# Kernel optimization log

Hardware: AMD Instinct MI355X
Metric: run time of the kernel (lower is better)

## Reference

```python
import jax, jax.numpy as jnp
import numpy as np

N_NODES = 100000
N_GRAPHS = 64


def gcn_conv(x, edge_index, edge_weight, W, b):
    # PyG GCNConv: h = W^T x, then out[dst] += norm * h[src], norm = d^-1/2[src]*w*d^-1/2[dst]
    n = x.shape[0]
    loop = jnp.arange(n)
    src = jnp.concatenate([edge_index[0], loop])
    dst = jnp.concatenate([edge_index[1], loop])
    w = jnp.concatenate([edge_weight, jnp.ones((n,), x.dtype)])  # self-loop weight 1
    deg = jax.ops.segment_sum(w, dst, num_segments=n)
    dis = jnp.where(deg > 0, jax.lax.rsqrt(jnp.maximum(deg, 1e-30)), 0.0)
    norm = dis[src] * w * dis[dst]                      # [E+N]
    h = x @ W                                            # [N, d_out]
    msg = h[src] * norm[:, None]                         # gather + scale
    out = jax.ops.segment_sum(msg, dst, num_segments=n)  # scatter-add
    return out + b


def setup_inputs() -> dict:
    key = jax.random.key(0)
    k = jax.random.split(key, 8)
    d_in, d_out = 256, 128
    E = 1600000
    x = jax.random.normal(k[0], (N_NODES, d_in), jnp.float32)
    edge_index = jax.random.randint(k[1], (2, E), 0, N_NODES, jnp.int64)
    edge_weight = jax.random.uniform(k[2], (E,), jnp.float32)
    batch = jnp.sort(jax.random.randint(k[3], (N_NODES,), 0, N_GRAPHS, jnp.int64))
    W_conv = jax.random.normal(k[4], (d_in, d_out), jnp.float32) / np.sqrt(d_in)
    b_conv = jnp.zeros((d_out,), jnp.float32)
    W_lin = jax.random.normal(k[5], (d_out, 1), jnp.float32) / np.sqrt(d_out)
    b_lin = jnp.zeros((1,), jnp.float32)
    return {"x": x, "edge_index": edge_index, "edge_weight": edge_weight,
            "batch": batch, "W_conv": W_conv, "b_conv": b_conv,
            "W_lin": W_lin, "b_lin": b_lin}


def reference(x, edge_index, edge_weight, batch, W_conv, b_conv, W_lin, b_lin):
    h = gcn_conv(x, edge_index, edge_weight, W_conv, b_conv)
    h = jax.nn.relu(h)
    # dropout(p=0.1) treated as identity (eval) for deterministic baseline
    sums = jax.ops.segment_sum(h, batch, num_segments=N_GRAPHS)
    counts = jax.ops.segment_sum(jnp.ones((h.shape[0],), h.dtype), batch,
                                 num_segments=N_GRAPHS)
    pooled = sums / jnp.maximum(counts, 1.0)[:, None]    # [G, d_out]
    logits = pooled @ W_lin + b_lin                       # [G, 1]
    return jax.nn.sigmoid(logits)
```

## Files before the change

kernel.cpp:

```cpp
#include <hip/hip_runtime.h>
#include <hip/hip_bf16.h>
#include <math.h>

#define D_IN 256
#define D_OUT 128
#define WSCALE 1073741824.0f

typedef __bf16 bf16x8 __attribute__((ext_vector_type(8)));
typedef float  f32x4  __attribute__((ext_vector_type(4)));

__device__ __forceinline__ float b2f(ushort u) {
    union { unsigned int i; float f; } v; v.i = ((unsigned int)u) << 16; return v.f;
}
__device__ __forceinline__ ushort f2b(float f) {
    unsigned int x = __float_as_uint(f);
    unsigned int r = (x + 0x7FFFu + ((x >> 16) & 1u)) >> 16;
    return (ushort)r;
}

__global__ void edge_k(const int* __restrict__ dst, const float* __restrict__ w,
                       unsigned long long* __restrict__ packed,
                       int* __restrict__ pos, int E) {
    int e = blockIdx.x * blockDim.x + threadIdx.x;
    if (e >= E) return;
    int d = dst[e];
    unsigned long long inc = (1ull << 40) |
        (unsigned long long)(w[e] * WSCALE);
    unsigned long long old = atomicAdd(&packed[d], inc);
    pos[e] = (int)(old >> 40);
}

__global__ __launch_bounds__(256) void scan1_k(const unsigned long long* __restrict__ packed,
                                               int* __restrict__ row_start,
                                               int* __restrict__ blksum,
                                               float* __restrict__ dis, int N) {
    __shared__ int sdata[256];
    int t = threadIdx.x;
    int base = blockIdx.x * 1024;
    int v[4], s = 0;
    #pragma unroll
    for (int i = 0; i < 4; ++i) {
        int idx = base + t * 4 + i;
        if (idx < N) {
            unsigned long long p = packed[idx];
            v[i] = (int)(p >> 40);
            float deg = 1.0f + (float)(p & ((1ull << 40) - 1)) * (1.0f / WSCALE);
            dis[idx] = rsqrtf(deg);
        } else v[i] = 0;
        s += v[i];
    }
    sdata[t] = s;
    __syncthreads();
    #pragma unroll
    for (int off = 1; off < 256; off <<= 1) {
        int x = 0;
        if (t >= off) x = sdata[t - off];
        __syncthreads();
        sdata[t] += x;
        __syncthreads();
    }
    int excl = sdata[t] - s;
    if (t == 255) blksum[blockIdx.x] = sdata[t];
    int run = excl;
    #pragma unroll
    for (int i = 0; i < 4; ++i) {
        int idx = base + t * 4 + i;
        if (idx < N) row_start[idx] = run;
        run += v[i];
    }
}

__global__ __launch_bounds__(256) void scan2_k(const int* __restrict__ blksum,
                                               int* __restrict__ blkpre,
                                               int NB, int* __restrict__ row_start, int N) {
    __shared__ int s[256];
    int t = threadIdx.x;
    int v = (t < NB) ? blksum[t] : 0;
    s[t] = v;
    __syncthreads();
    #pragma unroll
    for (int off = 1; off < 256; off <<= 1) {
        int x = 0;
        if (t >= off) x = s[t - off];
        __syncthreads();
        s[t] += x;
        __syncthreads();
    }
    if (t < NB) blkpre[t] = s[t] - v;
    if (t == 255) row_start[N] = s[255];
}

__global__ void scan3_k(int* __restrict__ row_start, const int* __restrict__ blkpre, int N) {
    int idx = blockIdx.x * blockDim.x + threadIdx.x;
    if (idx < N) row_start[idx] += blkpre[idx >> 10];
}

__global__ void fill_k(const int* __restrict__ src, const int* __restrict__ dst,
                       const float* __restrict__ w, const int* __restrict__ pos,
                       const int* __restrict__ row_start,
                       int2* __restrict__ csr, int E) {
    int e = blockIdx.x * blockDim.x + threadIdx.x;
    if (e >= E) return;
    int d = dst[e];
    int2 rec;
    rec.x = src[e];
    rec.y = __float_as_int(w[e]);
    csr[row_start[d] + pos[e]] = rec;
}

__global__ void wt_k(const float* __restrict__ W, ushort* __restrict__ Wtg) {
    int t = blockIdx.x * 256 + threadIdx.x;
    if (t < D_IN * D_OUT) {
        int k = t >> 7, n = t & 127;
        Wtg[n * D_IN + k] = f2b(W[t]);
    }
}

__global__ __launch_bounds__(256, 2) void gemm_k(const float* __restrict__ X,
                                                 const ushort* __restrict__ Wtg,
                                                 const float* __restrict__ dis,
                                                 ushort* __restrict__ H, int M) {
    extern __shared__ char smem[];
    const int t = threadIdx.x;
    const int brow = blockIdx.x * 128;
    const int wid = t >> 6;
    const int lane = t & 63;
    const int lrow = lane & 15;
    const int lkc = lane >> 4;

    bf16x8 breg[2][8];
    #pragma unroll
    for (int n = 0; n < 2; ++n) {
        int col = wid * 32 + n * 16 + lrow;
        const char* base = (const char*)(Wtg + col * D_IN);
        #pragma unroll
        for (int kk = 0; kk < 8; ++kk)
            breg[n][kk] = *(const bf16x8*)(base + kk * 64 + lkc * 16);
    }

    {
        const float4* x4 = (const float4*)X;
        #pragma unroll
        for (int i = 0; i < 32; ++i) {
            int f = t + 256 * i;
            int row = f >> 6;
            int c4 = f & 63;
            int gr = brow + row;
            if (gr > M - 1) gr = M - 1;
            float4 v = x4[(size_t)gr * 64 + c4];
            ushort4 u;
            u.x = f2b(v.x); u.y = f2b(v.y); u.z = f2b(v.z); u.w = f2b(v.w);
            int phys = row * 512 + (((c4 >> 1) ^ (row & 7)) << 4) + ((c4 & 1) << 3);
            *(ushort4*)(smem + phys) = u;
        }
    }
    __syncthreads();

    f32x4 acc[8][2];
    #pragma unroll
    for (int m = 0; m < 8; ++m)
        #pragma unroll
        for (int n = 0; n < 2; ++n) acc[m][n] = (f32x4){0.f, 0.f, 0.f, 0.f};

    #pragma unroll
    for (int kk = 0; kk < 8; ++kk) {
        bf16x8 a[8];
        #pragma unroll
        for (int m = 0; m < 8; ++m) {
            int row = m * 16 + lrow;
            int chunk = kk * 4 + lkc;
            a[m] = *(const bf16x8*)(smem + row * 512 + ((chunk ^ (row & 7)) << 4));
        }
        #pragma unroll
        for (int m = 0; m < 8; ++m) {
            acc[m][0] = __builtin_amdgcn_mfma_f32_16x16x32_bf16(a[m], breg[0][kk], acc[m][0], 0, 0, 0);
            acc[m][1] = __builtin_amdgcn_mfma_f32_16x16x32_bf16(a[m], breg[1][kk], acc[m][1], 0, 0, 0);
        }
    }

    #pragma unroll
    for (int m = 0; m < 8; ++m) {
        #pragma unroll
        for (int v = 0; v < 4; ++v) {
            int gr = brow + m * 16 + lkc * 4 + v;
            if (gr < M) {
                float dsc = dis[gr];
                size_t rb = (size_t)gr * D_OUT;
                H[rb + wid * 32 + lrow]      = f2b(dsc * acc[m][0][v]);
                H[rb + wid * 32 + 16 + lrow] = f2b(dsc * acc[m][1][v]);
            }
        }
    }
}

__global__ __launch_bounds__(256) void agg_pool_k(const int* __restrict__ row_start,
                                                  const int2* __restrict__ csr,
                                                  const ushort* __restrict__ h,
                                                  const float* __restrict__ dis,
                                                  const float* __restrict__ bconv,
                                                  const int* __restrict__ batch,
                                                  float* __restrict__ pooled,
                                                  float* __restrict__ counts, int N) {
    int wave = threadIdx.x >> 6;
    int lane = threadIdx.x & 63;
    int c = lane * 2;
    float2 b2 = *(const float2*)&bconv[c];
    int base = blockIdx.x * 64 + wave;

    float2 accp = make_float2(0.f, 0.f);
    int curg = -1;
    float gcount = 0.f;

    #pragma unroll 1
    for (int i = 0; i < 16; ++i) {
        int n = base + 4 * i;
        if (n >= N) break;
        int rs = row_start[n];
        int re = row_start[n + 1];
        float din = dis[n];
        ushort2 hu = *(const ushort2*)&h[(size_t)n * D_OUT + c];
        float ax = b2f(hu.x);
        float ay = b2f(hu.y);
        int j = rs;
        for (; j + 3 < re; j += 4) {
            int2 r0 = csr[j];
            int2 r1 = csr[j + 1];
            int2 r2 = csr[j + 2];
            int2 r3 = csr[j + 3];
            ushort2 u0 = *(const ushort2*)&h[(size_t)r0.x * D_OUT + c];
            ushort2 u1 = *(const ushort2*)&h[(size_t)r1.x * D_OUT + c];
            ushort2 u2 = *(const ushort2*)&h[(size_t)r2.x * D_OUT + c];
            ushort2 u3 = *(const ushort2*)&h[(size_t)r3.x * D_OUT + c];
            float n0 = __int_as_float(r0.y), n1 = __int_as_float(r1.y);
            float n2 = __int_as_float(r2.y), n3 = __int_as_float(r3.y);
            ax += n0 * b2f(u0.x) + n1 * b2f(u1.x) + n2 * b2f(u2.x) + n3 * b2f(u3.x);
            ay += n0 * b2f(u0.y) + n1 * b2f(u1.y) + n2 * b2f(u2.y) + n3 * b2f(u3.y);
        }
        for (; j < re; ++j) {
            int2 r0 = csr[j];
            ushort2 u0 = *(const ushort2*)&h[(size_t)r0.x * D_OUT + c];
            float n0 = __int_as_float(r0.y);
            ax += n0 * b2f(u0.x);
            ay += n0 * b2f(u0.y);
        }
        float vx = fmaxf(din * ax + b2.x, 0.f);
        float vy = fmaxf(din * ay + b2.y, 0.f);
        int g = batch[n];
        if (g != curg) {
            if (curg >= 0) {
                atomicAdd(&pooled[curg * D_OUT + c],     accp.x);
                atomicAdd(&pooled[curg * D_OUT + c + 1], accp.y);
                if (lane == 0) atomicAdd(&counts[curg], gcount);
            }
            accp = make_float2(0.f, 0.f);
            gcount = 0.f;
            curg = g;
        }
        accp.x += vx;
        accp.y += vy;
        gcount += 1.f;
    }
    if (curg >= 0) {
        atomicAdd(&pooled[curg * D_OUT + c],     accp.x);
        atomicAdd(&pooled[curg * D_OUT + c + 1], accp.y);
        if (lane == 0) atomicAdd(&counts[curg], gcount);
    }
}

__global__ void head_k(const float* __restrict__ pooled, const float* __restrict__ counts,
                       const float* __restrict__ wlin, const float* __restrict__ blin,
                       float* __restrict__ out, int G) {
    int g = blockIdx.x;
    int lane = threadIdx.x;
    float s = 0.f;
    for (int c = lane; c < D_OUT; c += 64)
        s += pooled[g * D_OUT + c] * wlin[c];
    #pragma unroll
    for (int off = 32; off; off >>= 1) s += __shfl_down(s, off);
    if (lane == 0) {
        float cnt = fmaxf(counts[g], 1.0f);
        float z = s / cnt + blin[0];
        out[g] = 1.0f / (1.0f + expf(-z));
    }
}

extern "C" void kernel_launch(void* const* d_in, const int* in_sizes, int n_in,
                              void* d_out, int out_size, void* d_ws, size_t ws_size,
                              hipStream_t stream) {
    const float* x     = (const float*)d_in[0];
    const int*   ei    = (const int*)  d_in[1];
    const float* ew    = (const float*)d_in[2];
    const int*   batch = (const int*)  d_in[3];
    const float* Wc    = (const float*)d_in[4];
    const float* bc    = (const float*)d_in[5];
    const float* Wl    = (const float*)d_in[6];
    const float* bl    = (const float*)d_in[7];
    float* out = (float*)d_out;

    const int E = in_sizes[2];
    const int N = in_sizes[3];
    const int G = out_size;
    const int NB = (N + 1023) >> 10;

    const int* src = ei;
    const int* dst = ei + E;

    unsigned long long* packed = (unsigned long long*)d_ws;
    float*  pooled   = (float*)(packed + N);
    float*  counts   = pooled + (size_t)G * D_OUT;
    int*    pos      = (int*)(counts + G);
    float*  dis      = (float*)(pos + E);
    ushort* h        = (ushort*)(dis + N);
    ushort* Wtg      = h + (size_t)N * D_OUT;
    int2*   csr      = (int2*)(Wtg + D_IN * D_OUT);
    int*    row_start= (int*)(csr + E);
    int*    blksum   = row_start + N + 1;
    int*    blkpre   = blksum + NB;

    size_t zbytes = (size_t)N * 8 + ((size_t)G * D_OUT + G) * sizeof(float);
    hipMemsetAsync(packed, 0, zbytes, stream);

    edge_k    <<<(E + 255) / 256, 256, 0, stream>>>(dst, ew, packed, pos, E);

    scan1_k   <<<NB, 256, 0, stream>>>(packed, row_start, blksum, dis, N);
    scan2_k   <<<1, 256, 0, stream>>>(blksum, blkpre, NB, row_start, N);
    scan3_k   <<<(N + 255) / 256, 256, 0, stream>>>(row_start, blkpre, N);

    fill_k    <<<(E + 255) / 256, 256, 0, stream>>>(src, dst, ew, pos, row_start, csr, E);

    wt_k      <<<(D_IN * D_OUT + 255) / 256, 256, 0, stream>>>(Wc, Wtg);
    gemm_k    <<<(N + 127) / 128, 256, 65536, stream>>>(x, Wtg, dis, h, N);

    agg_pool_k<<<(N + 63) / 64, 256, 0, stream>>>(row_start, csr, h, dis, bc, batch, pooled, counts, N);

    head_k    <<<G, 64, 0, stream>>>(pooled, counts, Wl, bl, out, G);
}
```

Before: 261.8 us.

## Fuse edge-degree atomics with GEMM and precompute full edge norms in CSR

Merges the edge degree-counting kernel and the GEMM into one launch whose leading blocks do the atomics and whose trailing blocks do the matmul, so the two independent stages overlap. The GEMM no longer scales rows by dis. The full symmetric norm dis[src]*w*dis[dst] is instead computed in fill_k and stored in the CSR record, and the self-loop is scaled by dis^2. The aggregation kernel now gives each wave 16 contiguous nodes, which improves batch-segment locality, and its edge loop gathers 8 neighbours at a time with masked tails. Costs include the dropped min-2-blocks launch bound on the GEMM and extra random dis gathers in fill_k.

```diff
diff --git a/kernel.cpp b/kernel.cpp
--- a/kernel.cpp
+++ b/kernel.cpp
@@ -16,96 +16,6 @@
     unsigned int x = __float_as_uint(f);
     unsigned int r = (x + 0x7FFFu + ((x >> 16) & 1u)) >> 16;
     return (ushort)r;
-}
-
-__global__ void edge_k(const int* __restrict__ dst, const float* __restrict__ w,
-                       unsigned long long* __restrict__ packed,
-                       int* __restrict__ pos, int E) {
-    int e = blockIdx.x * blockDim.x + threadIdx.x;
-    if (e >= E) return;
-    int d = dst[e];
-    unsigned long long inc = (1ull << 40) |
-        (unsigned long long)(w[e] * WSCALE);
-    unsigned long long old = atomicAdd(&packed[d], inc);
-    pos[e] = (int)(old >> 40);
-}
-
-__global__ __launch_bounds__(256) void scan1_k(const unsigned long long* __restrict__ packed,
-                                               int* __restrict__ row_start,
-                                               int* __restrict__ blksum,
-                                               float* __restrict__ dis, int N) {
-    __shared__ int sdata[256];
-    int t = threadIdx.x;
-    int base = blockIdx.x * 1024;
-    int v[4], s = 0;
-    #pragma unroll
-    for (int i = 0; i < 4; ++i) {
-        int idx = base + t * 4 + i;
-        if (idx < N) {
-            unsigned long long p = packed[idx];
-            v[i] = (int)(p >> 40);
-            float deg = 1.0f + (float)(p & ((1ull << 40) - 1)) * (1.0f / WSCALE);
-            dis[idx] = rsqrtf(deg);
-        } else v[i] = 0;
-        s += v[i];
-    }
-    sdata[t] = s;
-    __syncthreads();
-    #pragma unroll
-    for (int off = 1; off < 256; off <<= 1) {
-        int x = 0;
-        if (t >= off) x = sdata[t - off];
-        __syncthreads();
-        sdata[t] += x;
-        __syncthreads();
-    }
-    int excl = sdata[t] - s;
-    if (t == 255) blksum[blockIdx.x] = sdata[t];
-    int run = excl;
-    #pragma unroll
-    for (int i = 0; i < 4; ++i) {
-        int idx = base + t * 4 + i;
-        if (idx < N) row_start[idx] = run;
-        run += v[i];
-    }
-}
-
-__global__ __launch_bounds__(256) void scan2_k(const int* __restrict__ blksum,
-                                               int* __restrict__ blkpre,
-                                               int NB, int* __restrict__ row_start, int N) {
-    __shared__ int s[256];
-    int t = threadIdx.x;
-    int v = (t < NB) ? blksum[t] : 0;
-    s[t] = v;
-    __syncthreads();
-    #pragma unroll
-    for (int off = 1; off < 256; off <<= 1) {
-        int x = 0;
-        if (t >= off) x = s[t - off];
-        __syncthreads();
-        s[t] += x;
-        __syncthreads();
-    }
-    if (t < NB) blkpre[t] = s[t] - v;
-    if (t == 255) row_start[N] = s[255];
-}
-
-__global__ void scan3_k(int* __restrict__ row_start, const int* __restrict__ blkpre, int N) {
-    int idx = blockIdx.x * blockDim.x + threadIdx.x;
-    if (idx < N) row_start[idx] += blkpre[idx >> 10];
-}
-
-__global__ void fill_k(const int* __restrict__ src, const int* __restrict__ dst,
-                       const float* __restrict__ w, const int* __restrict__ pos,
-                       const int* __restrict__ row_start,
-                       int2* __restrict__ csr, int E) {
-    int e = blockIdx.x * blockDim.x + threadIdx.x;
-    if (e >= E) return;
-    int d = dst[e];
-    int2 rec;
-    rec.x = src[e];
-    rec.y = __float_as_int(w[e]);
-    csr[row_start[d] + pos[e]] = rec;
 }
 
 __global__ void wt_k(const float* __restrict__ W, ushort* __restrict__ Wtg) {
@@ -116,13 +26,27 @@
     }
 }
 
-__global__ __launch_bounds__(256, 2) void gemm_k(const float* __restrict__ X,
-                                                 const ushort* __restrict__ Wtg,
-                                                 const float* __restrict__ dis,
-                                                 ushort* __restrict__ H, int M) {
+__global__ __launch_bounds__(256) void fused_k(const int* __restrict__ dst,
+                                               const float* __restrict__ w,
+                                               unsigned long long* __restrict__ packed,
+                                               int* __restrict__ pos, int E, int EB,
+                                               const float* __restrict__ X,
+                                               const ushort* __restrict__ Wtg,
+                                               ushort* __restrict__ H, int M) {
+    if (blockIdx.x < (unsigned)EB) {
+        int e = blockIdx.x * 256 + threadIdx.x;
+        if (e < E) {
+            int d = dst[e];
+            unsigned long long inc = (1ull << 40) |
+                (unsigned long long)(w[e] * WSCALE);
+            unsigned long long old = atomicAdd(&packed[d], inc);
+            pos[e] = (int)(old >> 40);
+        }
+        return;
+    }
     extern __shared__ char smem[];
     const int t = threadIdx.x;
-    const int brow = blockIdx.x * 128;
+    const int brow = (blockIdx.x - EB) * 128;
     const int wid = t >> 6;
     const int lane = t & 63;
     const int lrow = lane & 15;
@@ -184,13 +108,92 @@
         for (int v = 0; v < 4; ++v) {
             int gr = brow + m * 16 + lkc * 4 + v;
             if (gr < M) {
-                float dsc = dis[gr];
                 size_t rb = (size_t)gr * D_OUT;
-                H[rb + wid * 32 + lrow]      = f2b(dsc * acc[m][0][v]);
-                H[rb + wid * 32 + 16 + lrow] = f2b(dsc * acc[m][1][v]);
+                H[rb + wid * 32 + lrow]      = f2b(acc[m][0][v]);
+                H[rb + wid * 32 + 16 + lrow] = f2b(acc[m][1][v]);
             }
         }
     }
+}
+
+__global__ __launch_bounds__(256) void scan1_k(const unsigned long long* __restrict__ packed,
+                                               int* __restrict__ row_start,
+                                               int* __restrict__ blksum,
+                                               float* __restrict__ dis, int N) {
+    __shared__ int sdata[256];
+    int t = threadIdx.x;
+    int base = blockIdx.x * 1024;
+    int v[4], s = 0;
+    #pragma unroll
+    for (int i = 0; i < 4; ++i) {
+        int idx = base + t * 4 + i;
+        if (idx < N) {
+            unsigned long long p = packed[idx];
+            v[i] = (int)(p >> 40);
+            float deg = 1.0f + (float)(p & ((1ull << 40) - 1)) * (1.0f / WSCALE);
+            dis[idx] = rsqrtf(deg);
+        } else v[i] = 0;
+        s += v[i];
+    }
+    sdata[t] = s;
+    __syncthreads();
+    #pragma unroll
+    for (int off = 1; off < 256; off <<= 1) {
+        int x = 0;
+        if (t >= off) x = sdata[t - off];
+        __syncthreads();
+        sdata[t] += x;
+        __syncthreads();
+    }
+    int excl = sdata[t] - s;
+    if (t == 255) blksum[blockIdx.x] = sdata[t];
+    int run = excl;
+    #pragma unroll
+    for (int i = 0; i < 4; ++i) {
+        int idx = base + t * 4 + i;
+        if (idx < N) row_start[idx] = run;
+        run += v[i];
+    }
+}
+
+__global__ __launch_bounds__(256) void scan2_k(const int* __restrict__ blksum,
+                                               int* __restrict__ blkpre,
+                                               int NB, int* __restrict__ row_start, int N) {
+    __shared__ int s[256];
+    int t = threadIdx.x;
+    int v = (t < NB) ? blksum[t] : 0;
+    s[t] = v;
+    __syncthreads();
+    #pragma unroll
+    for (int off = 1; off < 256; off <<= 1) {
+        int x = 0;
+        if (t >= off) x = s[t - off];
+        __syncthreads();
+        s[t] += x;
+        __syncthreads();
+    }
+    if (t < NB) blkpre[t] = s[t] - v;
+    if (t == 255) row_start[N] = s[255];
+}
+
+__global__ void scan3_k(int* __restrict__ row_start, const int* __restrict__ blkpre, int N) {
+    int idx = blockIdx.x * blockDim.x + threadIdx.x;
+    if (idx < N) row_start[idx] += blkpre[idx >> 10];
+}
+
+__global__ void fill_k(const int* __restrict__ src, const int* __restrict__ dst,
+                       const float* __restrict__ w, const int* __restrict__ pos,
+                       const int* __restrict__ row_start, const float* __restrict__ dis,
+                       int2* __restrict__ csr, int E) {
+    int e = blockIdx.x * blockDim.x + threadIdx.x;
+    if (e >= E) return;
+    int s = src[e];
+    int d = dst[e];
+    float nm = dis[s] * w[e] * dis[d];
+    int2 rec;
+    rec.x = s;
+    rec.y = __float_as_int(nm);
+    csr[row_start[d] + pos[e]] = rec;
 }
 
 __global__ __launch_bounds__(256) void agg_pool_k(const int* __restrict__ row_start,
@@ -205,46 +208,47 @@
     int lane = threadIdx.x & 63;
     int c = lane * 2;
     float2 b2 = *(const float2*)&bconv[c];
-    int base = blockIdx.x * 64 + wave;
+    int n0 = (blockIdx.x * 4 + wave) * 16;
 
     float2 accp = make_float2(0.f, 0.f);
     int curg = -1;
     float gcount = 0.f;
 
+    int nend = n0 + 16;
+    if (nend > N) nend = N;
+
     #pragma unroll 1
-    for (int i = 0; i < 16; ++i) {
-        int n = base + 4 * i;
-        if (n >= N) break;
+    for (int n = n0; n < nend; ++n) {
         int rs = row_start[n];
         int re = row_start[n + 1];
         float din = dis[n];
         ushort2 hu = *(const ushort2*)&h[(size_t)n * D_OUT + c];
-        float ax = b2f(hu.x);
-        float ay = b2f(hu.y);
-        int j = rs;
-        for (; j + 3 < re; j += 4) {
-            int2 r0 = csr[j];
-            int2 r1 = csr[j + 1];
-            int2 r2 = csr[j + 2];
-            int2 r3 = csr[j + 3];
-            ushort2 u0 = *(const ushort2*)&h[(size_t)r0.x * D_OUT + c];
-            ushort2 u1 = *(const ushort2*)&h[(size_t)r1.x * D_OUT + c];
-            ushort2 u2 = *(const ushort2*)&h[(size_t)r2.x * D_OUT + c];
-            ushort2 u3 = *(const ushort2*)&h[(size_t)r3.x * D_OUT + c];
-            float n0 = __int_as_float(r0.y), n1 = __int_as_float(r1.y);
-            float n2 = __int_as_float(r2.y), n3 = __int_as_float(r3.y);
-            ax += n0 * b2f(u0.x) + n1 * b2f(u1.x) + n2 * b2f(u2.x) + n3 * b2f(u3.x);
-            ay += n0 * b2f(u0.y) + n1 * b2f(u1.y) + n2 * b2f(u2.y) + n3 * b2f(u3.y);
-        }
-        for (; j < re; ++j) {
-            int2 r0 = csr[j];
-            ushort2 u0 = *(const ushort2*)&h[(size_t)r0.x * D_OUT + c];
-            float n0 = __int_as_float(r0.y);
-            ax += n0 * b2f(u0.x);
-            ay += n0 * b2f(u0.y);
-        }
-        float vx = fmaxf(din * ax + b2.x, 0.f);
-        float vy = fmaxf(din * ay + b2.y, 0.f);
+        float dn2 = din * din;
+        float ax = dn2 * b2f(hu.x);
+        float ay = dn2 * b2f(hu.y);
+        #pragma unroll 1
+        for (int j = rs; j < re; j += 8) {
+            int   idx[8];
+            float nm[8];
+            #pragma unroll
+            for (int k = 0; k < 8; ++k) {
+                int jj = j + k;
+                int2 r = csr[jj < re ? jj : re - 1];
+                idx[k] = r.x;
+                nm[k] = (jj < re) ? __int_as_float(r.y) : 0.f;
+            }
+            ushort2 uu[8];
+            #pragma unroll
+            for (int k = 0; k < 8; ++k)
+                uu[k] = *(const ushort2*)&h[(size_t)idx[k] * D_OUT + c];
+            #pragma unroll
+            for (int k = 0; k < 8; ++k) {
+                ax += nm[k] * b2f(uu[k].x);
+                ay += nm[k] * b2f(uu[k].y);
+            }
+        }
+        float vx = fmaxf(ax + b2.x, 0.f);
+        float vy = fmaxf(ay + b2.y, 0.f);
         int g = batch[n];
         if (g != curg) {
             if (curg >= 0) {
@@ -301,6 +305,8 @@
     const int N = in_sizes[3];
     const int G = out_size;
     const int NB = (N + 1023) >> 10;
+    const int EB = (E + 255) / 256;
+    const int GB = (N + 127) / 128;
 
     const int* src = ei;
     const int* dst = ei + E;
@@ -320,16 +326,16 @@
     size_t zbytes = (size_t)N * 8 + ((size_t)G * D_OUT + G) * sizeof(float);
     hipMemsetAsync(packed, 0, zbytes, stream);
 
-    edge_k    <<<(E + 255) / 256, 256, 0, stream>>>(dst, ew, packed, pos, E);
+    wt_k      <<<(D_IN * D_OUT + 255) / 256, 256, 0, stream>>>(Wc, Wtg);
+
+    fused_k   <<<EB + GB, 256, 65536, stream>>>(dst, ew, packed, pos, E, EB,
+                                                x, Wtg, h, N);
 
     scan1_k   <<<NB, 256, 0, stream>>>(packed, row_start, blksum, dis, N);
     scan2_k   <<<1, 256, 0, stream>>>(blksum, blkpre, NB, row_start, N);
     scan3_k   <<<(N + 255) / 256, 256, 0, stream>>>(row_start, blkpre, N);
 
-    fill_k    <<<(E + 255) / 256, 256, 0, stream>>>(src, dst, ew, pos, row_start, csr, E);
-
-    wt_k      <<<(D_IN * D_OUT + 255) / 256, 256, 0, stream>>>(Wc, Wtg);
-    gemm_k    <<<(N + 127) / 128, 256, 65536, stream>>>(x, Wtg, dis, h, N);
+    fill_k    <<<(E + 255) / 256, 256, 0, stream>>>(src, dst, ew, pos, row_start, dis, csr, E);
 
     agg_pool_k<<<(N + 63) / 64, 256, 0, stream>>>(row_start, csr, h, dis, bc, batch, pooled, counts, N);
 
```

New measurement: 266.0 us. Within noise of the previous version (+1.6%).
